# Kernel optimization log

Measured on AMD Instinct MI355X. Metric: run time of the kernel, lower is better.

## Reference

```python
import jax, jax.numpy as jnp
import numpy as np

NUM_HEADS = 8
DIM_HEAD = 64
EMBED = NUM_HEADS * DIM_HEAD  # 512
B, S, L = 2, 128, 128


def setup_inputs() -> dict:
    key = jax.random.key(0)
    k1, k2 = jax.random.split(key)
    x = jax.random.normal(k1, (B, EMBED, S, L), dtype=jnp.float32)
    # 1x1 Conv2d == pointwise linear over channels: weight [3E, E], bias [3E]
    W = jax.random.normal(k2, (3 * EMBED, EMBED), dtype=jnp.float32) * (EMBED ** -0.5)
    b = jnp.zeros((3 * EMBED,), dtype=jnp.float32)
    return {"x": x, "W": W, "b": b}


def reference(x, W, b):
    Bsz, D, S_, L_ = x.shape
    H, Dh = NUM_HEADS, DIM_HEAD
    scale = Dh ** -0.5
    # QKV projection (1x1 conv)
    qkv = jnp.einsum('oi,bisl->bosl', W, x) + b[None, :, None, None]
    q, k, v = jnp.split(qkv, 3, axis=1)
    q = q.reshape(Bsz, H, Dh, S_, L_) * scale
    k = k.reshape(Bsz, H, Dh, S_, L_)
    v = v.reshape(Bsz, H, Dh, S_, L_)
    # Column attention: attend along S axis, independently per column l
    col_scores = jnp.einsum('bhdsl,bhdtl->bhlst', q, k)      # [B,H,L,S,S]
    col_attn = jax.nn.softmax(col_scores, axis=-1)
    out_col = jnp.einsum('bhlst,bhdtl->bhdsl', col_attn, v)  # [B,H,Dh,S,L]
    # Row attention: attend along L axis, independently per row s
    row_scores = jnp.einsum('bhdsl,bhdsm->bhslm', q, k)      # [B,H,S,L,L]
    row_attn = jax.nn.softmax(row_scores, axis=-1)
    out_row = jnp.einsum('bhslm,bhdsm->bhdsl', row_attn, v)  # [B,H,Dh,S,L]
    out = (out_col + out_row).reshape(Bsz, H * Dh, S_, L_)
    return out
```

## Files before the change

kernel.cpp:

```cpp
#include <hip/hip_runtime.h>
#include <stdint.h>

#define EMB 512
#define THREE_E 1536
#define SL 16384
#define K_DIM 512

typedef unsigned short ushort;
typedef short bf16x8 __attribute__((ext_vector_type(8)));
typedef float f32x4 __attribute__((ext_vector_type(4)));

__device__ __forceinline__ ushort f2bf(float f) {
  unsigned u = __float_as_uint(f);
  u += 0x7fffu + ((u >> 16) & 1u);
  return (ushort)(u >> 16);
}
__device__ __forceinline__ float bf2f(ushort s) {
  return __uint_as_float((unsigned)s << 16);
}

__global__ __launch_bounds__(256) void wconv(const float* __restrict__ W,
                                             ushort* __restrict__ Wb) {
  int i = blockIdx.x * 256 + threadIdx.x;
  float4 f = ((const float4*)W)[i];
  uint2 o;
  o.x = (unsigned)f2bf(f.x) | ((unsigned)f2bf(f.y) << 16);
  o.y = (unsigned)f2bf(f.z) | ((unsigned)f2bf(f.w) << 16);
  ((uint2*)Wb)[i] = o;
}

__global__ __launch_bounds__(256) void xpose(const float* __restrict__ x,
                                             ushort* __restrict__ xT) {
  __shared__ ushort t[64][65];
  int b = blockIdx.z;
  int i0 = blockIdx.y * 64;
  int n0 = blockIdx.x * 64;
  int c = threadIdx.x & 63;
  int r0 = threadIdx.x >> 6;
  const float* xp = x + ((size_t)(b * EMB + i0)) * SL + n0;
  #pragma unroll
  for (int rr = 0; rr < 16; rr++) {
    int r = r0 * 16 + rr;
    t[r][c] = f2bf(xp[(size_t)r * SL + c]);
  }
  __syncthreads();
  ushort* op = xT + ((size_t)(b * SL + n0)) * EMB + i0;
  #pragma unroll
  for (int rr = 0; rr < 16; rr++) {
    int rn = r0 * 16 + rr;
    op[(size_t)rn * EMB + c] = t[c][rn];
  }
}

__global__ __launch_bounds__(256) void qkv_gemm(const ushort* __restrict__ Wb,
                                                const ushort* __restrict__ xT,
                                                const float* __restrict__ bias,
                                                ushort* __restrict__ rowQ) {
  __shared__ __align__(16) char sm[34816];
  ushort* As = (ushort*)sm;
  ushort* Bs = (ushort*)(sm + 8192);
  const int tid = threadIdx.x;
  const int b = blockIdx.z;
  const int m0 = blockIdx.y * 128;
  const int n0 = blockIdx.x * 128;
  const int lane = tid & 63;
  const int w = tid >> 6;
  const int wr = (w >> 1) * 64;
  const int wc = (w & 1) * 64;
  const int l15 = lane & 15;
  const int quad = lane >> 4;
  const int q8 = quad * 8;
  const ushort* xb = xT + (size_t)b * SL * EMB;
  f32x4 acc[4][4] = {};
  const int rowA = tid >> 2;
  const int cbA = (tid & 3) << 3;
  for (int k0 = 0; k0 < K_DIM; k0 += 32) {
    __syncthreads();
    *(uint4*)&As[rowA * 32 + cbA]        = *(const uint4*)&Wb[(size_t)(m0 + rowA) * K_DIM + k0 + cbA];
    *(uint4*)&As[(rowA + 64) * 32 + cbA] = *(const uint4*)&Wb[(size_t)(m0 + rowA + 64) * K_DIM + k0 + cbA];
    *(uint4*)&Bs[rowA * 32 + cbA]        = *(const uint4*)&xb[(size_t)(n0 + rowA) * K_DIM + k0 + cbA];
    *(uint4*)&Bs[(rowA + 64) * 32 + cbA] = *(const uint4*)&xb[(size_t)(n0 + rowA + 64) * K_DIM + k0 + cbA];
    __syncthreads();
    bf16x8 av[4], bv[4];
    #pragma unroll
    for (int mt = 0; mt < 4; mt++)
      av[mt] = *(const bf16x8*)&As[(wr + mt * 16 + l15) * 32 + q8];
    #pragma unroll
    for (int nt = 0; nt < 4; nt++)
      bv[nt] = *(const bf16x8*)&Bs[(wc + nt * 16 + l15) * 32 + q8];
    #pragma unroll
    for (int mt = 0; mt < 4; mt++)
      #pragma unroll
      for (int nt = 0; nt < 4; nt++)
        acc[mt][nt] = __builtin_amdgcn_mfma_f32_16x16x32_bf16(av[mt], bv[nt], acc[mt][nt], 0, 0, 0);
  }
  __syncthreads();
  {
    ushort* epi = (ushort*)sm;
    const float sc = (m0 < EMB) ? 0.125f : 1.0f;
    const int q4r = quad * 4;
    #pragma unroll
    for (int mt = 0; mt < 4; mt++) {
      int mb = wr + mt * 16 + q4r;
      float b0 = bias[m0 + mb], b1 = bias[m0 + mb + 1];
      float b2 = bias[m0 + mb + 2], b3 = bias[m0 + mb + 3];
      #pragma unroll
      for (int nt = 0; nt < 4; nt++) {
        int l = wc + nt * 16 + l15;
        unsigned u0 = f2bf((acc[mt][nt][0] + b0) * sc);
        unsigned u1 = f2bf((acc[mt][nt][1] + b1) * sc);
        unsigned u2 = f2bf((acc[mt][nt][2] + b2) * sc);
        unsigned u3 = f2bf((acc[mt][nt][3] + b3) * sc);
        uint2 pk;
        pk.x = u0 | (u1 << 16);
        pk.y = u2 | (u3 << 16);
        *(uint2*)&epi[l * 136 + mb] = pk;
      }
    }
  }
  __syncthreads();
  {
    const ushort* epi = (const ushort*)sm;
    const int sel = m0 >> 9;
    const int hb = (m0 & 511) >> 6;
    const int s = blockIdx.x;
    #pragma unroll
    for (int it = 0; it < 8; it++) {
      int flat = it * 2048 + tid * 8;
      int head = flat >> 13;
      int rem = flat & 8191;
      int l = rem >> 6;
      int dd = rem & 63;
      size_t dst = ((((size_t)(b * 3 + sel) * 8 + hb + head) * 128 + s) * 128 + l) * 64 + dd;
      *(uint4*)&rowQ[dst] = *(const uint4*)&epi[l * 136 + head * 64 + dd];
    }
  }
}

__global__ __launch_bounds__(256) void attn2(const ushort* __restrict__ qkv,
                                             ushort* __restrict__ tmp,
                                             float* __restrict__ out,
                                             int colpass) {
  __shared__ ushort Qs[128 * 72];
  __shared__ ushort Ks[128 * 72];
  __shared__ ushort Vt[64 * 136];
  __shared__ ushort Ps[64 * 136];
  __shared__ ushort Os[64 * 72];
  const int tid = threadIdx.x;
  const int fixed = blockIdx.x;
  const int h = blockIdx.y, b = blockIdx.z;
  const int w = tid >> 6, lane = tid & 63, l15 = lane & 15, quad = lane >> 4;
  const size_t off = colpass ? (size_t)fixed * 64 : (size_t)fixed * 8192;
  const size_t tstr = colpass ? 8192 : 64;
  const ushort* Qg = qkv + ((size_t)(b * 3 + 0) * 8 + h) * 1048576 + off;
  const ushort* Kg = Qg + (size_t)8 * 1048576;
  const ushort* Vg = Qg + (size_t)16 * 1048576;
  ushort* tb = tmp + (size_t)(b * 8 + h) * 1048576;
  {
    int trow = tid >> 3, d0 = (tid & 7) * 8, dg = tid & 7;
    #pragma unroll
    for (int it = 0; it < 4; it++) {
      int t = trow + it * 32;
      size_t g = (size_t)t * tstr + d0;
      *(uint4*)&Qs[t * 72 + d0] = *(const uint4*)&Qg[g];
      *(uint4*)&Ks[t * 72 + d0] = *(const uint4*)&Kg[g];
      uint4 vv = *(const uint4*)&Vg[g];
      ushort* vs = (ushort*)&vv;
      #pragma unroll
      for (int k = 0; k < 8; k++) {
        int i = (k + dg) & 7;
        Vt[(d0 + i) * 136 + t] = vs[i];
      }
    }
  }
  __syncthreads();
  for (int c = 0; c < 2; c++) {
    if (!colpass) {
      #pragma unroll
      for (int it = 0; it < 2; it++) {
        int flat = (it * 256 + tid) * 8;
        int row = flat >> 6, dd = flat & 63;
        *(uint4*)&Os[row * 72 + dd] =
            *(const uint4*)&tb[(size_t)(c * 64 + row) * 8192 + (size_t)fixed * 64 + dd];
      }
    }
    const int sb = c * 64 + w * 16;
    bf16x8 aq0 = *(const bf16x8*)&Qs[(sb + l15) * 72 + quad * 8];
    bf16x8 aq1 = *(const bf16x8*)&Qs[(sb + l15) * 72 + 32 + quad * 8];
    f32x4 accS[8];
    #pragma unroll
    for (int nt = 0; nt < 8; nt++) {
      f32x4 z = {0.f, 0.f, 0.f, 0.f};
      bf16x8 bk0 = *(const bf16x8*)&Ks[(nt * 16 + l15) * 72 + quad * 8];
      bf16x8 bk1 = *(const bf16x8*)&Ks[(nt * 16 + l15) * 72 + 32 + quad * 8];
      z = __builtin_amdgcn_mfma_f32_16x16x32_bf16(aq0, bk0, z, 0, 0, 0);
      z = __builtin_amdgcn_mfma_f32_16x16x32_bf16(aq1, bk1, z, 0, 0, 0);
      accS[nt] = z;
    }
    float inv[4];
    #pragma unroll
    for (int r = 0; r < 4; r++) {
      float mx = accS[0][r];
      #pragma unroll
      for (int nt = 1; nt < 8; nt++) mx = fmaxf(mx, accS[nt][r]);
      mx = fmaxf(mx, __shfl_xor(mx, 1));
      mx = fmaxf(mx, __shfl_xor(mx, 2));
      mx = fmaxf(mx, __shfl_xor(mx, 4));
      mx = fmaxf(mx, __shfl_xor(mx, 8));
      float s = 0.f;
      #pragma unroll
      for (int nt = 0; nt < 8; nt++) {
        float p = __builtin_amdgcn_exp2f((accS[nt][r] - mx) * 1.44269504088896f);
        accS[nt][r] = p;
        s += p;
      }
      s += __shfl_xor(s, 1);
      s += __shfl_xor(s, 2);
      s += __shfl_xor(s, 4);
      s += __shfl_xor(s, 8);
      inv[r] = 1.0f / s;
    }
    #pragma unroll
    for (int nt = 0; nt < 8; nt++)
      #pragma unroll
      for (int r = 0; r < 4; r++)
        Ps[(w * 16 + quad * 4 + r) * 136 + nt * 16 + l15] = f2bf(accS[nt][r]);
    __syncthreads();
    f32x4 accO[4] = {{0.f,0.f,0.f,0.f},{0.f,0.f,0.f,0.f},{0.f,0.f,0.f,0.f},{0.f,0.f,0.f,0.f}};
    #pragma unroll
    for (int kf = 0; kf < 4; kf++) {
      bf16x8 ap = *(const bf16x8*)&Ps[(w * 16 + l15) * 136 + kf * 32 + quad * 8];
      #pragma unroll
      for (int nt = 0; nt < 4; nt++) {
        bf16x8 bv = *(const bf16x8*)&Vt[(nt * 16 + l15) * 136 + kf * 32 + quad * 8];
        accO[nt] = __builtin_amdgcn_mfma_f32_16x16x32_bf16(ap, bv, accO[nt], 0, 0, 0);
      }
    }
    if (colpass) {
      #pragma unroll
      for (int nt = 0; nt < 4; nt++)
        #pragma unroll
        for (int r = 0; r < 4; r++)
          Os[(w * 16 + quad * 4 + r) * 72 + nt * 16 + l15] = f2bf(accO[nt][r] * inv[r]);
      __syncthreads();
      #pragma unroll
      for (int it = 0; it < 2; it++) {
        int flat = (it * 256 + tid) * 8;
        *(uint4*)&tb[(size_t)fixed * 8192 + c * 4096 + flat] =
            *(const uint4*)&Os[(flat >> 6) * 72 + (flat & 63)];
      }
      __syncthreads();
    } else {
      #pragma unroll
      for (int nt = 0; nt < 4; nt++)
        #pragma unroll
        for (int r = 0; r < 4; r++) {
          int row = w * 16 + quad * 4 + r, col = nt * 16 + l15;
          float v = accO[nt][r] * inv[r] + bf2f(Os[row * 72 + col]);
          Os[row * 72 + col] = f2bf(v);
        }
      __syncthreads();
      float* ob = out + (size_t)(b * EMB + h * 64) * SL + (size_t)fixed * 128 + c * 64;
      #pragma unroll
      for (int it = 0; it < 4; it++) {
        int f4 = it * 256 + tid;
        int d = f4 >> 4, l4 = f4 & 15;
        float4 o;
        o.x = bf2f(Os[(l4 * 4 + 0) * 72 + d]);
        o.y = bf2f(Os[(l4 * 4 + 1) * 72 + d]);
        o.z = bf2f(Os[(l4 * 4 + 2) * 72 + d]);
        o.w = bf2f(Os[(l4 * 4 + 3) * 72 + d]);
        *(float4*)&ob[(size_t)d * SL + l4 * 4] = o;
      }
      __syncthreads();
    }
  }
}

extern "C" void kernel_launch(void* const* d_in, const int* in_sizes, int n_in,
                              void* d_out, int out_size, void* d_ws, size_t ws_size,
                              hipStream_t stream) {
  const float* x = (const float*)d_in[0];
  const float* W = (const float*)d_in[1];
  const float* bias = (const float*)d_in[2];
  float* out = (float*)d_out;
  ushort* rowQ = (ushort*)d_ws;
  ushort* xT = (ushort*)((char*)d_ws + 100663296);
  ushort* tmp = (ushort*)((char*)d_ws + 100663296);
  ushort* Wb = (ushort*)((char*)d_ws + 134217728);

  hipLaunchKernelGGL(wconv, dim3(768), dim3(256), 0, stream, W, Wb);
  hipLaunchKernelGGL(xpose, dim3(256, 8, 2), dim3(256), 0, stream, x, xT);
  hipLaunchKernelGGL(qkv_gemm, dim3(128, 12, 2), dim3(256), 0, stream, Wb, xT, bias, rowQ);
  hipLaunchKernelGGL(attn2, dim3(128, 8, 2), dim3(256), 0, stream, rowQ, tmp, out, 1);
  hipLaunchKernelGGL(attn2, dim3(128, 8, 2), dim3(256), 0, stream, rowQ, tmp, out, 0);
}
```

Baseline: 297.3 us.

## Use async global-to-LDS loads with XOR swizzle in QKV GEMM; alias attention LDS buffers

The QKV GEMM now loads W and x tiles with global_load_lds directly into a swizzled LDS layout. K-steps are 64 wide instead of 32, which halves the number of barriers per tile and is meant to avoid LDS bank conflicts on the fragment reads. In the attention kernel, the row-pass partial from the column pass is read straight into registers instead of staged through LDS. Os now aliases the Ps buffer, which cuts LDS use so more blocks can be resident, at the cost of an extra barrier per chunk.

```diff
diff --git a/kernel.cpp b/kernel.cpp
--- a/kernel.cpp
+++ b/kernel.cpp
@@ -17,6 +17,12 @@
 }
 __device__ __forceinline__ float bf2f(ushort s) {
   return __uint_as_float((unsigned)s << 16);
+}
+
+__device__ __forceinline__ void async16(const ushort* g, ushort* l) {
+  __builtin_amdgcn_global_load_lds(
+      (const __attribute__((address_space(1))) unsigned int*)g,
+      (__attribute__((address_space(3))) unsigned int*)l, 16, 0, 0);
 }
 
 __global__ __launch_bounds__(256) void wconv(const float* __restrict__ W,
@@ -58,7 +64,7 @@
                                                 ushort* __restrict__ rowQ) {
   __shared__ __align__(16) char sm[34816];
   ushort* As = (ushort*)sm;
-  ushort* Bs = (ushort*)(sm + 8192);
+  ushort* Bs = (ushort*)(sm + 16384);
   const int tid = threadIdx.x;
   const int b = blockIdx.z;
   const int m0 = blockIdx.y * 128;
@@ -69,30 +75,39 @@
   const int wc = (w & 1) * 64;
   const int l15 = lane & 15;
   const int quad = lane >> 4;
-  const int q8 = quad * 8;
   const ushort* xb = xT + (size_t)b * SL * EMB;
   f32x4 acc[4][4] = {};
-  const int rowA = tid >> 2;
-  const int cbA = (tid & 3) << 3;
-  for (int k0 = 0; k0 < K_DIM; k0 += 32) {
-    __syncthreads();
-    *(uint4*)&As[rowA * 32 + cbA]        = *(const uint4*)&Wb[(size_t)(m0 + rowA) * K_DIM + k0 + cbA];
-    *(uint4*)&As[(rowA + 64) * 32 + cbA] = *(const uint4*)&Wb[(size_t)(m0 + rowA + 64) * K_DIM + k0 + cbA];
-    *(uint4*)&Bs[rowA * 32 + cbA]        = *(const uint4*)&xb[(size_t)(n0 + rowA) * K_DIM + k0 + cbA];
-    *(uint4*)&Bs[(rowA + 64) * 32 + cbA] = *(const uint4*)&xb[(size_t)(n0 + rowA + 64) * K_DIM + k0 + cbA];
-    __syncthreads();
-    bf16x8 av[4], bv[4];
-    #pragma unroll
-    for (int mt = 0; mt < 4; mt++)
-      av[mt] = *(const bf16x8*)&As[(wr + mt * 16 + l15) * 32 + q8];
-    #pragma unroll
-    for (int nt = 0; nt < 4; nt++)
-      bv[nt] = *(const bf16x8*)&Bs[(wc + nt * 16 + l15) * 32 + q8];
-    #pragma unroll
-    for (int mt = 0; mt < 4; mt++)
-      #pragma unroll
-      for (int nt = 0; nt < 4; nt++)
-        acc[mt][nt] = __builtin_amdgcn_mfma_f32_16x16x32_bf16(av[mt], bv[nt], acc[mt][nt], 0, 0, 0);
+  const int r8 = lane >> 3;
+  const int cg = (lane & 7) ^ r8;
+  for (int k0 = 0; k0 < K_DIM; k0 += 64) {
+    __syncthreads();
+    #pragma unroll
+    for (int t = 0; t < 4; t++) {
+      int seg = 4 * w + t;
+      int row = seg * 8 + r8;
+      async16(&Wb[(size_t)(m0 + row) * K_DIM + k0 + cg * 8], &As[seg * 512]);
+      async16(&xb[(size_t)(n0 + row) * K_DIM + k0 + cg * 8], &Bs[seg * 512]);
+    }
+    __syncthreads();
+    #pragma unroll
+    for (int ks = 0; ks < 2; ks++) {
+      bf16x8 av[4], bv[4];
+      #pragma unroll
+      for (int mt = 0; mt < 4; mt++) {
+        int row = wr + mt * 16 + l15;
+        av[mt] = *(const bf16x8*)&As[row * 64 + (((ks * 4 + quad) ^ (row & 7)) * 8)];
+      }
+      #pragma unroll
+      for (int nt = 0; nt < 4; nt++) {
+        int row = wc + nt * 16 + l15;
+        bv[nt] = *(const bf16x8*)&Bs[row * 64 + (((ks * 4 + quad) ^ (row & 7)) * 8)];
+      }
+      #pragma unroll
+      for (int mt = 0; mt < 4; mt++)
+        #pragma unroll
+        for (int nt = 0; nt < 4; nt++)
+          acc[mt][nt] = __builtin_amdgcn_mfma_f32_16x16x32_bf16(av[mt], bv[nt], acc[mt][nt], 0, 0, 0);
+    }
   }
   __syncthreads();
   {
@@ -144,8 +159,9 @@
   __shared__ ushort Qs[128 * 72];
   __shared__ ushort Ks[128 * 72];
   __shared__ ushort Vt[64 * 136];
-  __shared__ ushort Ps[64 * 136];
-  __shared__ ushort Os[64 * 72];
+  __shared__ ushort PsU[64 * 136];
+  ushort* Ps = PsU;
+  ushort* Os = PsU;
   const int tid = threadIdx.x;
   const int fixed = blockIdx.x;
   const int h = blockIdx.y, b = blockIdx.z;
@@ -174,15 +190,16 @@
     }
   }
   __syncthreads();
+  const int row0 = w * 16 + quad * 4;
   for (int c = 0; c < 2; c++) {
+    ushort treg[16];
     if (!colpass) {
-      #pragma unroll
-      for (int it = 0; it < 2; it++) {
-        int flat = (it * 256 + tid) * 8;
-        int row = flat >> 6, dd = flat & 63;
-        *(uint4*)&Os[row * 72 + dd] =
-            *(const uint4*)&tb[(size_t)(c * 64 + row) * 8192 + (size_t)fixed * 64 + dd];
-      }
+      const ushort* tp = tb + (size_t)(c * 64 + row0) * 8192 + (size_t)fixed * 64 + l15;
+      #pragma unroll
+      for (int r = 0; r < 4; r++)
+        #pragma unroll
+        for (int nt = 0; nt < 4; nt++)
+          treg[r * 4 + nt] = tp[(size_t)r * 8192 + nt * 16];
     }
     const int sb = c * 64 + w * 16;
     bf16x8 aq0 = *(const bf16x8*)&Qs[(sb + l15) * 72 + quad * 8];
@@ -224,7 +241,7 @@
     for (int nt = 0; nt < 8; nt++)
       #pragma unroll
       for (int r = 0; r < 4; r++)
-        Ps[(w * 16 + quad * 4 + r) * 136 + nt * 16 + l15] = f2bf(accS[nt][r]);
+        Ps[(row0 + r) * 136 + nt * 16 + l15] = f2bf(accS[nt][r]);
     __syncthreads();
     f32x4 accO[4] = {{0.f,0.f,0.f,0.f},{0.f,0.f,0.f,0.f},{0.f,0.f,0.f,0.f},{0.f,0.f,0.f,0.f}};
     #pragma unroll
@@ -236,30 +253,24 @@
         accO[nt] = __builtin_amdgcn_mfma_f32_16x16x32_bf16(ap, bv, accO[nt], 0, 0, 0);
       }
     }
+    __syncthreads();
+    #pragma unroll
+    for (int nt = 0; nt < 4; nt++)
+      #pragma unroll
+      for (int r = 0; r < 4; r++) {
+        float v = accO[nt][r] * inv[r];
+        if (!colpass) v += bf2f(treg[r * 4 + nt]);
+        Os[(row0 + r) * 72 + nt * 16 + l15] = f2bf(v);
+      }
+    __syncthreads();
     if (colpass) {
-      #pragma unroll
-      for (int nt = 0; nt < 4; nt++)
-        #pragma unroll
-        for (int r = 0; r < 4; r++)
-          Os[(w * 16 + quad * 4 + r) * 72 + nt * 16 + l15] = f2bf(accO[nt][r] * inv[r]);
-      __syncthreads();
       #pragma unroll
       for (int it = 0; it < 2; it++) {
         int flat = (it * 256 + tid) * 8;
         *(uint4*)&tb[(size_t)fixed * 8192 + c * 4096 + flat] =
             *(const uint4*)&Os[(flat >> 6) * 72 + (flat & 63)];
       }
-      __syncthreads();
     } else {
-      #pragma unroll
-      for (int nt = 0; nt < 4; nt++)
-        #pragma unroll
-        for (int r = 0; r < 4; r++) {
-          int row = w * 16 + quad * 4 + r, col = nt * 16 + l15;
-          float v = accO[nt][r] * inv[r] + bf2f(Os[row * 72 + col]);
-          Os[row * 72 + col] = f2bf(v);
-        }
-      __syncthreads();
       float* ob = out + (size_t)(b * EMB + h * 64) * SL + (size_t)fixed * 128 + c * 64;
       #pragma unroll
       for (int it = 0; it < 4; it++) {
@@ -272,8 +283,8 @@
         o.w = bf2f(Os[(l4 * 4 + 3) * 72 + d]);
         *(float4*)&ob[(size_t)d * SL + l4 * 4] = o;
       }
-      __syncthreads();
-    }
+    }
+    __syncthreads();
   }
 }
 
```

Result: faster. 290.3 us (-2.4%).
